# Optimization experiments

Measured on AMD Instinct MI355X. Metric: run time of the kernel, lower is better.

The kernel has to match this reference:

```python
import jax, jax.numpy as jnp
import numpy as np

B, L, A, D, H = 4, 1024, 8, 1024, 16
DK = D // H


def setup_inputs() -> dict:
    key = jax.random.key(0)
    ks = jax.random.split(key, 11)
    s = 1.0 / np.sqrt(D)
    return {
        "query": jax.random.normal(ks[0], (B, L, A, D), jnp.float32),
        "key": jax.random.normal(ks[1], (B, L, A, D), jnp.float32),
        "value": jax.random.normal(ks[2], (B, L, A, D), jnp.float32),
        "Wq": jax.random.uniform(ks[3], (D, D), jnp.float32, -s, s),
        "bq": jax.random.uniform(ks[4], (D,), jnp.float32, -s, s),
        "Wk": jax.random.uniform(ks[5], (D, D), jnp.float32, -s, s),
        "bk": jax.random.uniform(ks[6], (D,), jnp.float32, -s, s),
        "Wv": jax.random.uniform(ks[7], (D, D), jnp.float32, -s, s),
        "bv": jax.random.uniform(ks[8], (D,), jnp.float32, -s, s),
        "Wo": jax.random.uniform(ks[9], (D, D), jnp.float32, -s, s),
        "bo": jax.random.uniform(ks[10], (D,), jnp.float32, -s, s),
        "d_atrbt": A,
    }


def _proj_heads(x, W, b, a):
    # torch nn.Linear: x @ W.T + b; then view [B, L, a, H, DK] and transpose(2,3)
    y = jnp.einsum("blad,ed->blae", x, W) + b
    nb, nl = y.shape[0], y.shape[1]
    return y.reshape(nb, nl, a, H, DK).transpose(0, 1, 3, 2, 4)  # [B, L, H, a, DK]


def reference(query, key, value, Wq, bq, Wk, bk, Wv, bv, Wo, bo, d_atrbt):
    a = d_atrbt
    q = _proj_heads(query, Wq, bq, a)
    k = _proj_heads(key, Wk, bk, a)
    v = _proj_heads(value, Wv, bv, a)
    # scaled dot-product attention over the attribute axis (size a) per token
    scores = jnp.einsum("blhad,blhed->blhae", q, k) / jnp.sqrt(jnp.asarray(DK, q.dtype))
    p = jax.nn.softmax(scores, axis=-1)  # [B, L, H, a, a]
    x = jnp.einsum("blhae,blhed->blhad", p, v)  # [B, L, H, a, DK]
    nb, nl = x.shape[0], x.shape[1]
    x = x.transpose(0, 1, 3, 2, 4).reshape(nb, nl, a, H * DK)  # [B, L, a, D]
    return jnp.einsum("blad,ed->blae", x, Wo) + bo
```

## Files before the change

### kernel.cpp

```cpp
#include <hip/hip_runtime.h>
#include <hip/hip_bf16.h>
#include <stdint.h>

typedef unsigned short u16;
typedef __bf16 bf16x8 __attribute__((ext_vector_type(8)));
typedef float f32x4 __attribute__((ext_vector_type(4)));

#define MROWS 32768
#define NDIM  1024
#define KDIM  1024
#define NKT   16
#define MHALF 16777216

__device__ __forceinline__ void gload_lds16(const void* g, void* l) {
  __builtin_amdgcn_global_load_lds(
      (__attribute__((address_space(1))) const void*)g,
      (__attribute__((address_space(3))) void*)l,
      16, 0, 0);
}

struct CvtArgs { const float* s[4]; u16* d[4]; };

__global__ __launch_bounds__(256) void cvt4_kernel(CvtArgs ca) {
  const int which = blockIdx.x >> 9;
  const float* s = ca.s[which];
  u16* d = ca.d[which];
  const int i = ((((int)blockIdx.x & 511) * 256) + (int)threadIdx.x) * 8;
  const float4 f0 = *(const float4*)(s + i);
  const float4 f1 = *(const float4*)(s + i + 4);
  bf16x8 h;
  h[0] = (__bf16)f0.x; h[1] = (__bf16)f0.y; h[2] = (__bf16)f0.z; h[3] = (__bf16)f0.w;
  h[4] = (__bf16)f1.x; h[5] = (__bf16)f1.y; h[6] = (__bf16)f1.z; h[7] = (__bf16)f1.w;
  *(bf16x8*)((void*)(d + i)) = h;
}

__global__ __launch_bounds__(256) void cvt_half_kernel(const float* __restrict__ s,
                                                       u16* __restrict__ d) {
  const int i = ((int)blockIdx.x * 256 + (int)threadIdx.x) * 8;
  const float4 f0 = *(const float4*)(s + i);
  const float4 f1 = *(const float4*)(s + i + 4);
  bf16x8 h;
  h[0] = (__bf16)f0.x; h[1] = (__bf16)f0.y; h[2] = (__bf16)f0.z; h[3] = (__bf16)f0.w;
  h[4] = (__bf16)f1.x; h[5] = (__bf16)f1.y; h[6] = (__bf16)f1.z; h[7] = (__bf16)f1.w;
  *(bf16x8*)((void*)(d + i)) = h;
}

template <bool OUT_F32>
__global__ __launch_bounds__(512, 2) void gemm_bt256(const u16* __restrict__ Ab,
                                                     const u16* __restrict__ Bw,
                                                     const float* __restrict__ bias,
                                                     void* __restrict__ Cv,
                                                     int byPerXcd) {
  __shared__ __align__(16) unsigned char As[2][32768];
  __shared__ __align__(16) unsigned char Bs[2][32768];

  const int bid = (int)blockIdx.x;
  const int xcd = bid & 7;
  const int within = bid >> 3;
  const int by = xcd * byPerXcd + (within >> 2);
  const int bx = within & 3;

  const int t = (int)threadIdx.x;
  const int lane = t & 63;
  const int wid = t >> 6;
  const int wm = wid >> 2;
  const int wn = wid & 3;
  const int fr = lane & 15;
  const int hi = lane >> 4;

  size_t aG[4], bG[4]; int aL[4], bL[4];
#pragma unroll
  for (int i = 0; i < 4; ++i) {
    const int idx = i * 512 + t;
    const int r = idx >> 3, ch = idx & 7;
    const size_t cswz = (size_t)((ch ^ (r & 7)) << 3);
    aG[i] = (size_t)(by * 256 + r) * KDIM + cswz;
    bG[i] = (size_t)(bx * 256 + r) * KDIM + cswz;
    aL[i] = bL[i] = (i * 512 + (t & ~63)) * 16;
  }

  int aRow[8], bRow[4], colx[2];
#pragma unroll
  for (int m = 0; m < 8; ++m) aRow[m] = (wm * 128 + m * 16 + fr) * 128;
#pragma unroll
  for (int n = 0; n < 4; ++n) bRow[n] = (wn * 64 + n * 16 + fr) * 128;
#pragma unroll
  for (int kk = 0; kk < 2; ++kk) colx[kk] = (((kk * 4 + hi) ^ (fr & 7)) << 4);

  f32x4 acc[8][4] = {};

#pragma unroll
  for (int i = 0; i < 4; ++i) {
    gload_lds16(Ab + aG[i], &As[0][aL[i]]);
    gload_lds16(Bw + bG[i], &Bs[0][bL[i]]);
  }

  for (int kt = 0; kt < NKT; ++kt) {
    const int cur = kt & 1, nxt = cur ^ 1;
    __syncthreads();

    bf16x8 bf0[4], a0[4];
#pragma unroll
    for (int n = 0; n < 4; ++n)
      bf0[n] = *(const bf16x8*)((const void*)&Bs[cur][bRow[n] + colx[0]]);
#pragma unroll
    for (int m = 0; m < 4; ++m)
      a0[m] = *(const bf16x8*)((const void*)&As[cur][aRow[m] + colx[0]]);

    if (kt + 1 < NKT) {
      const int ko = (kt + 1) * 64;
#pragma unroll
      for (int i = 0; i < 4; ++i) {
        gload_lds16(Ab + aG[i] + ko, &As[nxt][aL[i]]);
        gload_lds16(Bw + bG[i] + ko, &Bs[nxt][bL[i]]);
      }
    }

    __builtin_amdgcn_s_setprio(1);
#pragma unroll
    for (int m = 0; m < 4; ++m)
#pragma unroll
      for (int n = 0; n < 4; ++n)
        acc[m][n] = __builtin_amdgcn_mfma_f32_16x16x32_bf16(a0[m], bf0[n], acc[m][n], 0, 0, 0);
    __builtin_amdgcn_s_setprio(0);
#pragma unroll
    for (int m = 0; m < 4; ++m)
      a0[m] = *(const bf16x8*)((const void*)&As[cur][aRow[4 + m] + colx[0]]);
    __builtin_amdgcn_s_setprio(1);
#pragma unroll
    for (int m = 0; m < 4; ++m)
#pragma unroll
      for (int n = 0; n < 4; ++n)
        acc[4 + m][n] = __builtin_amdgcn_mfma_f32_16x16x32_bf16(a0[m], bf0[n], acc[4 + m][n], 0, 0, 0);
    __builtin_amdgcn_s_setprio(0);

#pragma unroll
    for (int n = 0; n < 4; ++n)
      bf0[n] = *(const bf16x8*)((const void*)&Bs[cur][bRow[n] + colx[1]]);
#pragma unroll
    for (int m = 0; m < 4; ++m)
      a0[m] = *(const bf16x8*)((const void*)&As[cur][aRow[m] + colx[1]]);
    __builtin_amdgcn_s_setprio(1);
#pragma unroll
    for (int m = 0; m < 4; ++m)
#pragma unroll
      for (int n = 0; n < 4; ++n)
        acc[m][n] = __builtin_amdgcn_mfma_f32_16x16x32_bf16(a0[m], bf0[n], acc[m][n], 0, 0, 0);
    __builtin_amdgcn_s_setprio(0);
#pragma unroll
    for (int m = 0; m < 4; ++m)
      a0[m] = *(const bf16x8*)((const void*)&As[cur][aRow[4 + m] + colx[1]]);
    __builtin_amdgcn_s_setprio(1);
#pragma unroll
    for (int m = 0; m < 4; ++m)
#pragma unroll
      for (int n = 0; n < 4; ++n)
        acc[4 + m][n] = __builtin_amdgcn_mfma_f32_16x16x32_bf16(a0[m], bf0[n], acc[4 + m][n], 0, 0, 0);
    __builtin_amdgcn_s_setprio(0);
  }

  const int row0 = by * 256 + wm * 128 + hi * 4;
  const int col0 = bx * 256 + wn * 64 + fr;
#pragma unroll
  for (int n = 0; n < 4; ++n) {
    const int gc = col0 + n * 16;
    const float bv = bias[gc];
#pragma unroll
    for (int m = 0; m < 8; ++m) {
#pragma unroll
      for (int j = 0; j < 4; ++j) {
        const size_t idx = (size_t)(row0 + m * 16 + j) * NDIM + (size_t)gc;
        const float val = acc[m][n][j] + bv;
        if constexpr (OUT_F32)
          ((float*)Cv)[idx] = val;
        else
          ((u16*)Cv)[idx] = __builtin_bit_cast(u16, (__bf16)val);
      }
    }
  }
}

__global__ __launch_bounds__(256) void attn_kernel(u16* __restrict__ qx,
                                                   const u16* __restrict__ kb,
                                                   const u16* __restrict__ vb) {
  __shared__ __align__(16) u16 qs[4][8][64];
  __shared__ __align__(16) u16 ks[4][8][64];
  __shared__ __align__(16) u16 vs[4][8][64];
  const int t = threadIdx.x;
  const int lane = t & 63;
  const int w = t >> 6;
  const int unit = blockIdx.x * 4 + w;
  const int bl = unit >> 4;
  const int h = unit & 15;
  const int row = lane >> 3;
  const int c8 = (lane & 7) * 8;
  const size_t goff = (size_t)bl * 8 * 1024 + (size_t)h * 64 + (size_t)row * 1024 + c8;

  *(int4*)((void*)&qs[w][row][c8]) = *(const int4*)((const void*)&qx[goff]);
  *(int4*)((void*)&ks[w][row][c8]) = *(const int4*)((const void*)&kb[goff]);
  *(int4*)((void*)&vs[w][row][c8]) = *(const int4*)((const void*)&vb[goff]);
  __syncthreads();

  const int a = row;
  const int e = lane & 7;
  float s = 0.f;
#pragma unroll
  for (int d8 = 0; d8 < 64; d8 += 8) {
    const bf16x8 qv = *(const bf16x8*)((const void*)&qs[w][a][d8]);
    const bf16x8 kv = *(const bf16x8*)((const void*)&ks[w][e][d8]);
#pragma unroll
    for (int j = 0; j < 8; ++j) s += (float)qv[j] * (float)kv[j];
  }
  s *= 0.125f;

  float mx = s;
#pragma unroll
  for (int o = 1; o < 8; o <<= 1) mx = fmaxf(mx, __shfl_xor(mx, o));
  float p = __expf(s - mx);
  float sum = p;
#pragma unroll
  for (int o = 1; o < 8; o <<= 1) sum += __shfl_xor(sum, o);
  p /= sum;

  float xo[8] = {};
#pragma unroll
  for (int e2 = 0; e2 < 8; ++e2) {
    const float pe = __shfl(p, (lane & 56) + e2);
    const bf16x8 vv = *(const bf16x8*)((const void*)&vs[w][e2][c8]);
#pragma unroll
    for (int j = 0; j < 8; ++j) xo[j] += pe * (float)vv[j];
  }
  bf16x8 hx;
#pragma unroll
  for (int j = 0; j < 8; ++j) hx[j] = (__bf16)xo[j];
  *(int4*)((void*)&qx[goff]) = __builtin_bit_cast(int4, hx);
}

extern "C" void kernel_launch(void* const* d_in, const int* in_sizes, int n_in,
                              void* d_out, int out_size, void* d_ws, size_t ws_size,
                              hipStream_t stream) {
  const float* query = (const float*)d_in[0];
  const float* key   = (const float*)d_in[1];
  const float* value = (const float*)d_in[2];
  const float* Wq = (const float*)d_in[3];
  const float* bq = (const float*)d_in[4];
  const float* Wk = (const float*)d_in[5];
  const float* bk = (const float*)d_in[6];
  const float* Wv = (const float*)d_in[7];
  const float* bv = (const float*)d_in[8];
  const float* Wo = (const float*)d_in[9];
  const float* bo = (const float*)d_in[10];
  (void)in_sizes; (void)n_in; (void)out_size; (void)ws_size;

  const size_t mn = (size_t)MROWS * (size_t)NDIM;

  u16* kb = (u16*)d_out;
  u16* vb = kb + mn;
  u16* qb = (u16*)d_ws;
  u16* Wqb = qb + mn;
  u16* Wkb = Wqb + 1048576;
  u16* Wvb = Wkb + 1048576;
  u16* Wob = Wvb + 1048576;
  u16* Abf = Wob + 1048576;

  CvtArgs ca;
  ca.s[0] = Wq; ca.s[1] = Wk; ca.s[2] = Wv; ca.s[3] = Wo;
  ca.d[0] = Wqb; ca.d[1] = Wkb; ca.d[2] = Wvb; ca.d[3] = Wob;
  cvt4_kernel<<<2048, 256, 0, stream>>>(ca);

  const float* srcs[3] = {key, value, query};
  const u16* wts[3] = {Wkb, Wvb, Wqb};
  const float* bss[3] = {bk, bv, bq};
  u16* outs[3] = {kb, vb, qb};
  for (int g = 0; g < 3; ++g) {
    for (int h = 0; h < 2; ++h) {
      cvt_half_kernel<<<8192, 256, 0, stream>>>(srcs[g] + (size_t)h * MHALF, Abf);
      gemm_bt256<false><<<256, 512, 0, stream>>>(
          Abf, wts[g], bss[g], (void*)(outs[g] + (size_t)h * MHALF), 8);
    }
  }

  attn_kernel<<<16384, 256, 0, stream>>>(qb, kb, vb);

  gemm_bt256<true><<<512, 512, 0, stream>>>(qb, Wob, bo, d_out, 16);
}
```

Before: 494.9 us.

## Rewrite GEMM as 8-phase ping-pong pipeline and merge K/V launches

Replaces the double-buffered GEMM main loop with an eight-phase schedule. A and B tiles are split into 128-row halves and each half is prefetched while MFMAs run on the other, with explicit s_barrier, sched_barrier and vmcnt/lgkmcnt waits. It also drops the half-size cvt+GEMM split for key and value, using the q workspace as a full-size bf16 staging buffer so each runs as one 512-block launch. The goal is to hide global-to-LDS latency better and cut launch count. The cost is more barriers per k-step and fragile hand-placed wait counts.

```diff
diff --git a/kernel.cpp b/kernel.cpp
--- a/kernel.cpp
+++ b/kernel.cpp
@@ -34,8 +34,8 @@
   *(bf16x8*)((void*)(d + i)) = h;
 }
 
-__global__ __launch_bounds__(256) void cvt_half_kernel(const float* __restrict__ s,
-                                                       u16* __restrict__ d) {
+__global__ __launch_bounds__(256) void cvt_kernel(const float* __restrict__ s,
+                                                  u16* __restrict__ d) {
   const int i = ((int)blockIdx.x * 256 + (int)threadIdx.x) * 8;
   const float4 f0 = *(const float4*)(s + i);
   const float4 f1 = *(const float4*)(s + i + 4);
@@ -45,14 +45,20 @@
   *(bf16x8*)((void*)(d + i)) = h;
 }
 
+#define SBAR0() __builtin_amdgcn_sched_barrier(0)
+#define PH_SYNC() do { SBAR0(); __builtin_amdgcn_s_barrier(); \
+    asm volatile("s_waitcnt lgkmcnt(0)" ::: "memory"); SBAR0(); } while (0)
+#define PH_END() do { SBAR0(); __builtin_amdgcn_s_barrier(); } while (0)
+#define VM4() asm volatile("s_waitcnt vmcnt(4)" ::: "memory")
+
 template <bool OUT_F32>
-__global__ __launch_bounds__(512, 2) void gemm_bt256(const u16* __restrict__ Ab,
-                                                     const u16* __restrict__ Bw,
-                                                     const float* __restrict__ bias,
-                                                     void* __restrict__ Cv,
-                                                     int byPerXcd) {
-  __shared__ __align__(16) unsigned char As[2][32768];
-  __shared__ __align__(16) unsigned char Bs[2][32768];
+__global__ __launch_bounds__(512, 2) void gemm8p(const u16* __restrict__ Ab,
+                                                 const u16* __restrict__ Bw,
+                                                 const float* __restrict__ bias,
+                                                 void* __restrict__ Cv,
+                                                 int byPerXcd) {
+  __shared__ __align__(16) unsigned char As[2][2][16384];
+  __shared__ __align__(16) unsigned char Bs[2][2][16384];
 
   const int bid = (int)blockIdx.x;
   const int xcd = bid & 7;
@@ -65,99 +71,132 @@
   const int wid = t >> 6;
   const int wm = wid >> 2;
   const int wn = wid & 3;
+  const int bh = wn >> 1;
   const int fr = lane & 15;
   const int hi = lane >> 4;
 
-  size_t aG[4], bG[4]; int aL[4], bL[4];
-#pragma unroll
-  for (int i = 0; i < 4; ++i) {
+  size_t gOff[2]; int lOff[2];
+#pragma unroll
+  for (int i = 0; i < 2; ++i) {
     const int idx = i * 512 + t;
     const int r = idx >> 3, ch = idx & 7;
-    const size_t cswz = (size_t)((ch ^ (r & 7)) << 3);
-    aG[i] = (size_t)(by * 256 + r) * KDIM + cswz;
-    bG[i] = (size_t)(bx * 256 + r) * KDIM + cswz;
-    aL[i] = bL[i] = (i * 512 + (t & ~63)) * 16;
-  }
-
-  int aRow[8], bRow[4], colx[2];
-#pragma unroll
-  for (int m = 0; m < 8; ++m) aRow[m] = (wm * 128 + m * 16 + fr) * 128;
-#pragma unroll
-  for (int n = 0; n < 4; ++n) bRow[n] = (wn * 64 + n * 16 + fr) * 128;
-#pragma unroll
-  for (int kk = 0; kk < 2; ++kk) colx[kk] = (((kk * 4 + hi) ^ (fr & 7)) << 4);
+    gOff[i] = (size_t)r * KDIM + (size_t)((ch ^ (r & 7)) << 3);
+    lOff[i] = (i * 512 + (t & ~63)) * 16;
+  }
+  const u16* Abase = Ab + (size_t)(by * 256) * KDIM;
+  const u16* Bbase = Bw + (size_t)(bx * 256) * KDIM;
+
+  auto SA = [&](int tile, int d, int h) {
+    const u16* s = Abase + (size_t)(h * 128) * KDIM + tile * 64;
+#pragma unroll
+    for (int i = 0; i < 2; ++i) gload_lds16(s + gOff[i], &As[d][h][lOff[i]]);
+  };
+  auto SB = [&](int tile, int d, int h) {
+    const u16* s = Bbase + (size_t)(h * 128) * KDIM + tile * 64;
+#pragma unroll
+    for (int i = 0; i < 2; ++i) gload_lds16(s + gOff[i], &Bs[d][h][lOff[i]]);
+  };
+
+  int aOff[8][2], bOff[4][2];
+#pragma unroll
+  for (int m = 0; m < 8; ++m)
+#pragma unroll
+    for (int ks = 0; ks < 2; ++ks)
+      aOff[m][ks] = (m * 16 + fr) * 128 + (((ks * 4 + hi) ^ (fr & 7)) << 4);
+#pragma unroll
+  for (int n = 0; n < 4; ++n)
+#pragma unroll
+    for (int ks = 0; ks < 2; ++ks)
+      bOff[n][ks] = ((wn & 1) * 64 + n * 16 + fr) * 128 + (((ks * 4 + hi) ^ (fr & 7)) << 4);
 
   f32x4 acc[8][4] = {};
-
-#pragma unroll
-  for (int i = 0; i < 4; ++i) {
-    gload_lds16(Ab + aG[i], &As[0][aL[i]]);
-    gload_lds16(Bw + bG[i], &Bs[0][bL[i]]);
-  }
-
-  for (int kt = 0; kt < NKT; ++kt) {
-    const int cur = kt & 1, nxt = cur ^ 1;
-    __syncthreads();
-
-    bf16x8 bf0[4], a0[4];
-#pragma unroll
-    for (int n = 0; n < 4; ++n)
-      bf0[n] = *(const bf16x8*)((const void*)&Bs[cur][bRow[n] + colx[0]]);
+  bf16x8 a[4], b[8];
+
+  const unsigned char* Am0 = &As[0][wm][0];
+  const unsigned char* Am1 = &As[1][wm][0];
+  const unsigned char* Bm0 = &Bs[0][bh][0];
+  const unsigned char* Bm1 = &Bs[1][bh][0];
+
+  auto LDA4_0 = [&](int mlo, int ks) {
+#pragma unroll
+    for (int i = 0; i < 4; ++i)
+      a[i] = *(const bf16x8*)((const void*)(Am0 + aOff[mlo + i][ks]));
+  };
+  auto LDA4_1 = [&](int mlo, int ks) {
+#pragma unroll
+    for (int i = 0; i < 4; ++i)
+      a[i] = *(const bf16x8*)((const void*)(Am1 + aOff[mlo + i][ks]));
+  };
+  auto LDB8_0 = [&]() {
+#pragma unroll
+    for (int ks = 0; ks < 2; ++ks)
+#pragma unroll
+      for (int n = 0; n < 4; ++n)
+        b[ks * 4 + n] = *(const bf16x8*)((const void*)(Bm0 + bOff[n][ks]));
+  };
+  auto LDB8_1 = [&]() {
+#pragma unroll
+    for (int ks = 0; ks < 2; ++ks)
+#pragma unroll
+      for (int n = 0; n < 4; ++n)
+        b[ks * 4 + n] = *(const bf16x8*)((const void*)(Bm1 + bOff[n][ks]));
+  };
+  auto MM = [&](int mlo, int bo) {
+    __builtin_amdgcn_s_setprio(1);
 #pragma unroll
     for (int m = 0; m < 4; ++m)
-      a0[m] = *(const bf16x8*)((const void*)&As[cur][aRow[m] + colx[0]]);
-
-    if (kt + 1 < NKT) {
-      const int ko = (kt + 1) * 64;
-#pragma unroll
-      for (int i = 0; i < 4; ++i) {
-        gload_lds16(Ab + aG[i] + ko, &As[nxt][aL[i]]);
-        gload_lds16(Bw + bG[i] + ko, &Bs[nxt][bL[i]]);
-      }
-    }
-
-    __builtin_amdgcn_s_setprio(1);
-#pragma unroll
-    for (int m = 0; m < 4; ++m)
 #pragma unroll
       for (int n = 0; n < 4; ++n)
-        acc[m][n] = __builtin_amdgcn_mfma_f32_16x16x32_bf16(a0[m], bf0[n], acc[m][n], 0, 0, 0);
+        acc[mlo + m][n] = __builtin_amdgcn_mfma_f32_16x16x32_bf16(
+            a[m], b[bo + n], acc[mlo + m][n], 0, 0, 0);
     __builtin_amdgcn_s_setprio(0);
-#pragma unroll
-    for (int m = 0; m < 4; ++m)
-      a0[m] = *(const bf16x8*)((const void*)&As[cur][aRow[4 + m] + colx[0]]);
-    __builtin_amdgcn_s_setprio(1);
-#pragma unroll
-    for (int m = 0; m < 4; ++m)
-#pragma unroll
-      for (int n = 0; n < 4; ++n)
-        acc[4 + m][n] = __builtin_amdgcn_mfma_f32_16x16x32_bf16(a0[m], bf0[n], acc[4 + m][n], 0, 0, 0);
-    __builtin_amdgcn_s_setprio(0);
-
-#pragma unroll
-    for (int n = 0; n < 4; ++n)
-      bf0[n] = *(const bf16x8*)((const void*)&Bs[cur][bRow[n] + colx[1]]);
-#pragma unroll
-    for (int m = 0; m < 4; ++m)
-      a0[m] = *(const bf16x8*)((const void*)&As[cur][aRow[m] + colx[1]]);
-    __builtin_amdgcn_s_setprio(1);
-#pragma unroll
-    for (int m = 0; m < 4; ++m)
-#pragma unroll
-      for (int n = 0; n < 4; ++n)
-        acc[m][n] = __builtin_amdgcn_mfma_f32_16x16x32_bf16(a0[m], bf0[n], acc[m][n], 0, 0, 0);
-    __builtin_amdgcn_s_setprio(0);
-#pragma unroll
-    for (int m = 0; m < 4; ++m)
-      a0[m] = *(const bf16x8*)((const void*)&As[cur][aRow[4 + m] + colx[1]]);
-    __builtin_amdgcn_s_setprio(1);
-#pragma unroll
-    for (int m = 0; m < 4; ++m)
-#pragma unroll
-      for (int n = 0; n < 4; ++n)
-        acc[4 + m][n] = __builtin_amdgcn_mfma_f32_16x16x32_bf16(a0[m], bf0[n], acc[4 + m][n], 0, 0, 0);
-    __builtin_amdgcn_s_setprio(0);
-  }
+  };
+
+  SB(0, 0, 0); SB(0, 0, 1); SA(0, 0, 0); SA(0, 0, 1);
+  SB(1, 1, 0); SB(1, 1, 1);
+  VM4(); SBAR0();
+  __builtin_amdgcn_s_barrier();
+
+  for (int j = 0; j < NKT / 2; ++j) {
+    const int T1 = 2 * j + 1;
+    const int T2 = (2 * j + 2 < NKT) ? 2 * j + 2 : NKT - 1;
+    const int T3 = (2 * j + 3 < NKT) ? 2 * j + 3 : NKT - 1;
+
+    LDB8_0(); LDA4_0(0, 0);
+    SA(T1, 1, 0);
+    PH_SYNC(); MM(0, 0); PH_END();
+
+    LDA4_0(4, 0);
+    SA(T1, 1, 1);
+    PH_SYNC(); MM(4, 0); PH_END();
+
+    LDA4_0(0, 1);
+    SB(T2, 0, 0);
+    PH_SYNC(); MM(0, 4); PH_END();
+
+    LDA4_0(4, 1);
+    SB(T2, 0, 1);
+    PH_SYNC(); MM(4, 4);
+    VM4(); PH_END();
+
+    LDB8_1(); LDA4_1(0, 0);
+    SA(T2, 0, 0);
+    PH_SYNC(); MM(0, 0); PH_END();
+
+    LDA4_1(4, 0);
+    SA(T2, 0, 1);
+    PH_SYNC(); MM(4, 0); PH_END();
+
+    LDA4_1(0, 1);
+    SB(T3, 1, 0);
+    PH_SYNC(); MM(0, 4); PH_END();
+
+    LDA4_1(4, 1);
+    SB(T3, 1, 1);
+    PH_SYNC(); MM(4, 4);
+    VM4(); PH_END();
+  }
+  asm volatile("s_waitcnt vmcnt(0)" ::: "memory");
 
   const int row0 = by * 256 + wm * 128 + hi * 4;
   const int col0 = bx * 256 + wn * 64 + fr;
@@ -168,9 +207,9 @@
 #pragma unroll
     for (int m = 0; m < 8; ++m) {
 #pragma unroll
-      for (int j = 0; j < 4; ++j) {
-        const size_t idx = (size_t)(row0 + m * 16 + j) * NDIM + (size_t)gc;
-        const float val = acc[m][n][j] + bv;
+      for (int jj = 0; jj < 4; ++jj) {
+        const size_t idx = (size_t)(row0 + m * 16 + jj) * NDIM + (size_t)gc;
+        const float val = acc[m][n][jj] + bv;
         if constexpr (OUT_F32)
           ((float*)Cv)[idx] = val;
         else
@@ -268,19 +307,16 @@
   ca.d[0] = Wqb; ca.d[1] = Wkb; ca.d[2] = Wvb; ca.d[3] = Wob;
   cvt4_kernel<<<2048, 256, 0, stream>>>(ca);
 
-  const float* srcs[3] = {key, value, query};
-  const u16* wts[3] = {Wkb, Wvb, Wqb};
-  const float* bss[3] = {bk, bv, bq};
-  u16* outs[3] = {kb, vb, qb};
-  for (int g = 0; g < 3; ++g) {
-    for (int h = 0; h < 2; ++h) {
-      cvt_half_kernel<<<8192, 256, 0, stream>>>(srcs[g] + (size_t)h * MHALF, Abf);
-      gemm_bt256<false><<<256, 512, 0, stream>>>(
-          Abf, wts[g], bss[g], (void*)(outs[g] + (size_t)h * MHALF), 8);
-    }
-  }
+  cvt_kernel<<<16384, 256, 0, stream>>>(key, qb);
+  gemm8p<false><<<512, 512, 0, stream>>>(qb, Wkb, bk, (void*)kb, 16);
+  cvt_kernel<<<16384, 256, 0, stream>>>(value, qb);
+  gemm8p<false><<<512, 512, 0, stream>>>(qb, Wvb, bv, (void*)vb, 16);
+  cvt_kernel<<<8192, 256, 0, stream>>>(query, Abf);
+  gemm8p<false><<<256, 512, 0, stream>>>(Abf, Wqb, bq, (void*)qb, 8);
+  cvt_kernel<<<8192, 256, 0, stream>>>(query + MHALF, Abf);
+  gemm8p<false><<<256, 512, 0, stream>>>(Abf, Wqb, bq, (void*)(qb + MHALF), 8);
 
   attn_kernel<<<16384, 256, 0, stream>>>(qb, kb, vb);
 
-  gemm_bt256<true><<<512, 512, 0, stream>>>(qb, Wob, bo, d_out, 16);
-}
+  gemm8p<true><<<512, 512, 0, stream>>>(qb, Wob, bo, d_out, 16);
+}
```

Measured after the change: 468.5 us. -5.3%, faster.
